# Kernel optimization log

Hardware: AMD Instinct MI355X
Metric: run time of the kernel (lower is better)

## Reference

```python
import jax, jax.numpy as jnp
import numpy as np

# Config (from init_kwargs 'knn')
QUEUE_SIZE = 65536   # K
FEAT_DIM = 256       # D
BATCH = 512          # N (eval_sampling = 1.0 -> all samples used)
NUM_KNNS = 200
NUM_CLASSES = 1000
TEMPERATURE = 0.07


def _l2norm(x):
    return x / jnp.sqrt(jnp.sum(x * x, axis=-1, keepdims=True) + 1e-12)


def setup_inputs() -> dict:
    key = jax.random.key(0)
    k1, k2, k3, k4 = jax.random.split(key, 4)
    features = _l2norm(jax.random.normal(k1, (BATCH, FEAT_DIM), jnp.float32))
    labels = jax.random.randint(k2, (BATCH,), 0, NUM_CLASSES, jnp.int32)
    queue_features = _l2norm(jax.random.normal(k3, (QUEUE_SIZE, FEAT_DIM), jnp.float32))
    queue_labels = jax.random.randint(k4, (QUEUE_SIZE,), 0, NUM_CLASSES, jnp.int32)
    return {
        "features": features,
        "labels": labels,
        "queue_features": queue_features,
        "queue_labels": queue_labels,
        "queue_ptr": 0,
    }


def reference(features, labels, queue_features, queue_labels, queue_ptr):
    # ---- kNN accuracy (train branch, eval_sampling=1.0) ----
    sim = jnp.einsum('nc,kc->nk', features, queue_features)           # [N, K]
    sim_w, sim_idx = jax.lax.top_k(sim, k=NUM_KNNS)                   # [N, Kn]
    sim_w = jnp.exp(sim_w / TEMPERATURE)
    sim_labels = queue_labels[sim_idx]                                # [N, Kn] (vmapped gather)
    # weighted one-hot vote, expressed as a scatter-add (same math,
    # avoids the [N, Kn, C] one-hot intermediate)
    n = features.shape[0]
    pred_scores = jnp.zeros((n, NUM_CLASSES), sim_w.dtype)
    pred_scores = pred_scores.at[jnp.arange(n)[:, None], sim_labels].add(sim_w)
    pred_labels = jnp.argmax(pred_scores, axis=-1)
    accuracy = jnp.mean((pred_labels == labels).astype(jnp.float32))

    # ---- queue update (single device: all_gather == identity) ----
    batch_size = features.shape[0]
    inds = (jnp.arange(batch_size) + queue_ptr) % QUEUE_SIZE  # original asserts divisibility
    new_queue_features = queue_features.at[inds].set(features)
    new_queue_labels = queue_labels.at[inds].set(labels)
    new_queue_ptr = (queue_ptr + batch_size) % QUEUE_SIZE

    return accuracy, new_queue_features, new_queue_labels, new_queue_ptr
```

## Files before the change

kernel.cpp:

```cpp
#include <hip/hip_runtime.h>
#include <math.h>

#define NQ     65536
#define DIM    256
#define NBATCH 512
#define KNN    200
#define NCLS   1000
#define TSELF  0.155f
#define TSELH  0.150f
#define EPSF   0.0041f

#define GM  128
#define GK  32
#define NTN (NQ / GM)
#define KSTEPS (DIM / GK)

typedef unsigned short u16;
typedef unsigned long long u64;
typedef __attribute__((ext_vector_type(8))) short short8;
typedef __attribute__((ext_vector_type(4))) float f32x4;


__device__ __forceinline__ u16 f2bf(float x) {
  unsigned u = __float_as_uint(x);
  return (u16)((u + 0x7FFFu + ((u >> 16) & 1u)) >> 16);
}
__device__ __forceinline__ void load_lds16(const void* g, void* l) {
  __builtin_amdgcn_global_load_lds(
      (const __attribute__((address_space(1))) unsigned int*)g,
      (__attribute__((address_space(3))) unsigned int*)l, 16, 0, 0);
}
__device__ __forceinline__ void store_f4u(float* p, float4 v) {
  p[0] = v.x;
  *(float2*)(p + 1) = make_float2(v.y, v.z);
  p[3] = v.w;
}

__global__ __launch_bounds__(256) void prep_copy_kernel(
    const float* __restrict__ feat, const int* __restrict__ labels,
    const float* __restrict__ qf, const int* __restrict__ ql,
    const int* __restrict__ qptr,
    u16* __restrict__ Bb, u16* __restrict__ Ab,
    int* __restrict__ flag, float* __restrict__ out)
{
  const int idx = blockIdx.x * 256 + threadIdx.x;
  const int ptr = qptr[0];
  const long long NFEAT = (long long)NQ * DIM;

  {
    float4 qv = ((const float4*)qf)[idx];
    int row = idx >> 6;
    int c4  = idx & 63;
    int d = (row - ptr) & (NQ - 1);
    float4 ov = qv;
    if (d < NBATCH) ov = ((const float4*)feat)[d * 64 + c4];
    store_f4u(out + 1 + 4 * (long long)idx, ov);

    ushort4 h;
    h.x = f2bf(qv.x); h.y = f2bf(qv.y); h.z = f2bf(qv.z); h.w = f2bf(qv.w);
    ((ushort4*)Bb)[idx] = h;
  }

  if (idx < NBATCH * DIM / 4) {
    float4 v = ((const float4*)feat)[idx];
    ushort4 h;
    h.x = f2bf(v.x); h.y = f2bf(v.y); h.z = f2bf(v.z); h.w = f2bf(v.w);
    ((ushort4*)Ab)[idx] = h;
  }

  if (idx < NQ) {
    int d = (idx - ptr) & (NQ - 1);
    int v = (d < NBATCH) ? labels[d] : ql[idx];
    out[1 + NFEAT + idx] = (float)v;
  }

  if (idx < NBATCH) flag[idx] = 0;
  if (idx == 0) {
    out[0] = 0.0f;
    out[1 + NFEAT + NQ] = (float)((ptr + NBATCH) & (NQ - 1));
  }
}

__global__ __launch_bounds__(256) void gemm_mfma(
    const u16* __restrict__ A, const u16* __restrict__ B,
    uint2* __restrict__ cand, int* __restrict__ cnt2,
    int* __restrict__ flag, int SLOT)
{
  __shared__ u16 sA[2][GM][GK];
  __shared__ u16 sB[2][GM][GK];
  __shared__ int lcnt[GM];

  const int tid  = threadIdx.x;
  const int wave = tid >> 6, lane = tid & 63;
  const int d  = blockIdx.x;
  const int bm = (d >> 3) & 3;
  const int bn = (d & 7) | ((d >> 5) << 3);

  for (int i = tid; i < GM; i += 256) lcnt[i] = 0;

  const u16* srcBase = ((wave < 2) ? (A + (size_t)bm * GM * DIM)
                                   : (B + (size_t)bn * GM * DIM))
                       + (size_t)(wave & 1) * 64 * DIM;
  const int kx = ((lane & 3) ^ ((lane >> 3) & 3)) * 8;
  const u16* src = srcBase + (lane >> 2) * DIM + kx;
  u16* dst0 = ((wave < 2) ? &sA[0][0][0] : &sB[0][0][0]) + (wave & 1) * 64 * GK;
  u16* dst1 = ((wave < 2) ? &sA[1][0][0] : &sB[1][0][0]) + (wave & 1) * 64 * GK;

  const int wm = (wave & 1) * 64, wn = (wave >> 1) * 64;
  const int fr = lane & 15;
  const int fq = lane >> 4;
  const int fqx = fq ^ ((fr >> 1) & 3);

  f32x4 acc[4][4] = {};

  {
    const u16* s = src;
#pragma unroll
    for (int g = 0; g < 4; ++g)
      load_lds16(s + g * 16 * DIM, dst0 + g * 512);
  }
  __syncthreads();

  for (int t = 0; t < KSTEPS; ++t) {
    const int cur = t & 1;
    if (t + 1 < KSTEPS) {
      const u16* s = src + (t + 1) * GK;
      u16* dl = cur ? dst0 : dst1;
#pragma unroll
      for (int g = 0; g < 4; ++g)
        load_lds16(s + g * 16 * DIM, dl + g * 512);
    }

    short8 a[4], b[4];
#pragma unroll
    for (int i = 0; i < 4; ++i) {
      a[i] = *(const short8*)&sA[cur][wm + i * 16 + fr][fqx * 8];
      b[i] = *(const short8*)&sB[cur][wn + i * 16 + fr][fqx * 8];
    }
#pragma unroll
    for (int i = 0; i < 4; ++i)
#pragma unroll
      for (int j = 0; j < 4; ++j)
        acc[i][j] = __builtin_amdgcn_mfma_f32_16x16x32_bf16(a[i], b[j], acc[i][j], 0, 0, 0);

    __syncthreads();
  }

  const int lrow0 = wm + fq * 4;
  const int ccol  = bn * GM + wn + fr;
#pragma unroll
  for (int i = 0; i < 4; ++i)
#pragma unroll
    for (int j = 0; j < 4; ++j)
#pragma unroll
      for (int r = 0; r < 4; ++r) {
        float v = acc[i][j][r];
        if (v > TSELF) {
          int lr  = lrow0 + i * 16 + r;
          int col = ccol + j * 16;
          int p = atomicAdd(&lcnt[lr], 1);
          if (p < SLOT)
            cand[((size_t)(bm * GM + lr) * NTN + bn) * SLOT + p] =
                make_uint2(__float_as_uint(v), (unsigned)col);
          else
            flag[bm * GM + lr] = 1;
        }
      }
  __syncthreads();
  if (tid < GM) {
    int c = lcnt[tid];
    cnt2[(size_t)(bm * GM + tid) * NTN + bn] = c < SLOT ? c : SLOT;
  }
}

#define NBSEL 2048
#define CCAP  2048
#define LCAP  1024
#define NT    512
#define NG    (NT / 8)
#define NWV   (NT / 64)
#define BINW  ((1.001f - TSELH) / (float)NBSEL)

__global__ __launch_bounds__(NT, 4) void select_kernel(
    const uint2* __restrict__ cand, const int* __restrict__ cnt2,
    const int* __restrict__ flag, const int* __restrict__ labels,
    const int* __restrict__ qlab, const float* __restrict__ qf,
    const float* __restrict__ feat, float* __restrict__ out,
    float inv_n, int SLOT)
{
  __shared__ int   hist[NBSEL];
  __shared__ int   seg[NT];
  __shared__ int   wtot[NWV];
  __shared__ float candV[CCAP];
  __shared__ int   candI[CCAP];
  __shared__ float votes[NCLS];
  __shared__ u64   ek[LCAP];
  __shared__ int   lst[LCAP];
  __shared__ float frow[DIM];
  __shared__ int   s_b, s_cnt, s_mb;
  __shared__ float s_chk;
  __shared__ u64   s_best;

  const int tid = threadIdx.x;
  const int row = blockIdx.x;

  bool fb = (flag[row] != 0);

  if (tid < DIM) frow[tid] = feat[(size_t)row * DIM + tid];
  for (int i = tid; i < NBSEL; i += NT) hist[i] = 0;
  for (int c = tid; c < NCLS; c += NT) votes[c] = 0.0f;
  if (tid == 0) { s_b = 0; s_cnt = 0; s_mb = 0; s_best = 0ull; s_chk = -1.0f; }
  __syncthreads();

  if (!fb) {
    const int*   rowcnt  = cnt2 + (size_t)row * NTN;
    const uint2* rowcand = cand + (size_t)row * NTN * SLOT;
    for (int t = tid; t < NTN; t += NT) {
      int c = rowcnt[t];
      if (c > 0) {
        int p = atomicAdd(&s_cnt, c);
        for (int k = 0; k < c; ++k) {
          if (p + k < CCAP) {
            uint2 e = rowcand[(size_t)t * SLOT + k];
            candV[p + k] = __uint_as_float(e.x);
            candI[p + k] = (int)e.y;
          }
        }
      }
    }
    __syncthreads();
    const int n = s_cnt;
    if (n < KNN || n > CCAP) fb = true;
    else {
      const float SSCALE = 1.0f / BINW;
      for (int i = tid; i < n; i += NT) {
        int b = (int)((candV[i] - TSELH) * SSCALE);
        b = b < 0 ? 0 : (b > NBSEL - 1 ? NBSEL - 1 : b);
        atomicAdd(&hist[b], 1);
      }
      __syncthreads();
      {
        int s = 0;
#pragma unroll
        for (int i = 0; i < NBSEL / NT; ++i) s += hist[tid * (NBSEL / NT) + i];
        const int ln = tid & 63, wv = tid >> 6;
        int acc = s;
#pragma unroll
        for (int off = 1; off < 64; off <<= 1) {
          int o = __shfl_down(acc, off, 64);
          if (ln + off < 64) acc += o;
        }
        if (ln == 0) wtot[wv] = acc;
        __syncthreads();
        int addv = 0;
        for (int w = wv + 1; w < NWV; ++w) addv += wtot[w];
        seg[tid] = acc + addv;
      }
      __syncthreads();
      { int run = (tid < NT - 1) ? seg[tid + 1] : 0;
        for (int i = tid * (NBSEL / NT) + NBSEL / NT - 1;
             i >= tid * (NBSEL / NT); --i) {
          run += hist[i];
          if (run >= KNN) { atomicMax(&s_b, i); break; }
        } }
      __syncthreads();
      const int bstarA = s_b;
      const float thresh = TSELH + (float)bstarA * BINW - 2.0f * EPSF;

      for (int i = tid; i < n; i += NT) {
        if (candV[i] >= thresh) {
          int p = atomicAdd(&s_mb, 1);
          if (p < LCAP) lst[p] = i;
        }
      }
      __syncthreads();
      const int nr = s_mb;
      if (nr > LCAP || nr < KNN) fb = true;
      else {
        const int sub = tid & 7;
        const int grp = tid >> 3;
        const float4* fr4 = (const float4*)frow;

        float4 b0[8];
        if (grp < nr) {
          const float4* qr = (const float4*)(qf + (size_t)candI[lst[grp]] * DIM);
#pragma unroll
          for (int it = 0; it < 8; ++it) b0[it] = qr[sub + it * 8];
        }
        for (int k = grp; k < nr; k += NG) {
          const int kn = k + NG;
          float4 b1[8];
          if (kn < nr) {
            const float4* qr = (const float4*)(qf + (size_t)candI[lst[kn]] * DIM);
#pragma unroll
            for (int it = 0; it < 8; ++it) b1[it] = qr[sub + it * 8];
          }
          float p = 0.0f;
#pragma unroll
          for (int it = 0; it < 8; ++it) {
            float4 a = fr4[sub + it * 8];
            p = fmaf(a.x, b0[it].x, p); p = fmaf(a.y, b0[it].y, p);
            p = fmaf(a.z, b0[it].z, p); p = fmaf(a.w, b0[it].w, p);
          }
          p += __shfl_xor(p, 1, 64);
          p += __shfl_xor(p, 2, 64);
          p += __shfl_xor(p, 4, 64);
          if (sub == 0) candV[lst[k]] = p;
#pragma unroll
          for (int it = 0; it < 8; ++it) b0[it] = b1[it];
        }
        __syncthreads();

        for (int e = tid; e < nr; e += NT) {
          int ci = lst[e];
          ek[e] = ((u64)__float_as_uint(candV[ci]) << 32) |
                  (u64)(0xFFFFFFFFu - (unsigned)candI[ci]);
        }
        __syncthreads();

        for (int e = tid; e < nr; e += NT) {
          u64 ke = ek[e];
          int rank = 0;
          for (int j = 0; j < nr; ++j) rank += (ek[j] > ke);
          if (rank < KNN) {
            float v = __uint_as_float((unsigned)(ke >> 32));
            int col = (int)(0xFFFFFFFFu - (unsigned)(ke & 0xFFFFFFFFull));
            atomicAdd(&votes[qlab[col]], expf(v * (1.0f / 0.07f)));
            if (rank == KNN - 1) s_chk = v;
          }
        }
        __syncthreads();
        if (s_chk < TSELF + EPSF) fb = true;
      }
    }
  }

  if (fb) {
    for (int i = tid; i < NBSEL; i += NT) hist[i] = 0;
    if (tid == 0) { s_b = 0; s_cnt = 0; }
    __syncthreads();

    for (int q = tid; q < NQ; q += NT) {
      const float4* qr = (const float4*)(qf + (size_t)q * DIM);
      const float4* fr = (const float4*)frow;
      float s = 0.0f;
#pragma unroll
      for (int t = 0; t < DIM / 4; ++t) {
        float4 a = fr[t], b = qr[t];
        s = fmaf(a.x, b.x, s); s = fmaf(a.y, b.y, s);
        s = fmaf(a.z, b.z, s); s = fmaf(a.w, b.w, s);
      }
      int bin = (int)((s + 1.0f) * (NBSEL * 0.5f));
      bin = bin < 0 ? 0 : (bin > NBSEL - 1 ? NBSEL - 1 : bin);
      atomicAdd(&hist[bin], 1);
    }
    __syncthreads();

    { int s = 0;
#pragma unroll
      for (int i = 0; i < NBSEL / NT; ++i) s += hist[tid * (NBSEL / NT) + i];
      seg[tid] = s; }
    __syncthreads();
    for (int off = 1; off < NT; off <<= 1) {
      int t = (tid + off < NT) ? seg[tid + off] : 0;
      __syncthreads();
      seg[tid] += t;
      __syncthreads();
    }
    { int run = (tid < NT - 1) ? seg[tid + 1] : 0;
      for (int i = tid * (NBSEL / NT) + NBSEL / NT - 1;
           i >= tid * (NBSEL / NT); --i) {
        run += hist[i];
        if (run >= KNN) { atomicMax(&s_b, i); break; }
      } }
    __syncthreads();
    const int bstar = s_b;

    for (int q = tid; q < NQ; q += NT) {
      const float4* qr = (const float4*)(qf + (size_t)q * DIM);
      const float4* fr = (const float4*)frow;
      float s = 0.0f;
#pragma unroll
      for (int t = 0; t < DIM / 4; ++t) {
        float4 a = fr[t], b = qr[t];
        s = fmaf(a.x, b.x, s); s = fmaf(a.y, b.y, s);
        s = fmaf(a.z, b.z, s); s = fmaf(a.w, b.w, s);
      }
      int bin = (int)((s + 1.0f) * (NBSEL * 0.5f));
      bin = bin < 0 ? 0 : (bin > NBSEL - 1 ? NBSEL - 1 : bin);
      if (bin >= bstar) {
        int p = atomicAdd(&s_cnt, 1);
        if (p < CCAP) { candV[p] = s; candI[p] = q; }
      }
    }
    __syncthreads();
    int m = s_cnt < CCAP ? s_cnt : CCAP;

    int P = 256; while (P < m) P <<= 1;
    for (int i = tid; i < P; i += NT)
      if (i >= m) { candV[i] = -INFINITY; candI[i] = 0x7fffffff; }
    __syncthreads();
    for (int k = 2; k <= P; k <<= 1) {
      for (int j = k >> 1; j > 0; j >>= 1) {
        for (int i = tid; i < P; i += NT) {
          int ixj = i ^ j;
          if (ixj > i) {
            float va = candV[i], vb = candV[ixj];
            int ia = candI[i], ib = candI[ixj];
            bool aFirst = (va > vb) || (va == vb && ia < ib);
            bool up = ((i & k) == 0);
            if (up ? !aFirst : aFirst) {
              candV[i] = vb; candV[ixj] = va;
              candI[i] = ib; candI[ixj] = ia;
            }
          }
        }
        __syncthreads();
      }
    }

    for (int c = tid; c < NCLS; c += NT) votes[c] = 0.0f;
    __syncthreads();
    for (int i = tid; i < KNN; i += NT)
      atomicAdd(&votes[qlab[candI[i]]], expf(candV[i] * (1.0f / 0.07f)));
    __syncthreads();
  }

  u64 key = 0ull;
  for (int c = tid; c < NCLS; c += NT) {
    u64 k2 = ((u64)__float_as_uint(votes[c]) << 32) |
             (u64)(0xFFFFFFFFu - (unsigned)c);
    if (k2 > key) key = k2;
  }
  for (int off = 32; off > 0; off >>= 1) {
    u64 o = __shfl_down(key, off, 64);
    if (o > key) key = o;
  }
  if ((tid & 63) == 0) atomicMax(&s_best, key);
  __syncthreads();
  if (tid == 0) {
    int cls = (int)(0xFFFFFFFFu - (unsigned)(s_best & 0xFFFFFFFFull));
    if (cls == labels[row]) atomicAdd(out, inv_n);
  }
}

extern "C" void kernel_launch(void* const* d_in, const int* in_sizes, int n_in,
                              void* d_out, int out_size, void* d_ws, size_t ws_size,
                              hipStream_t stream)
{
  const float* features = (const float*)d_in[0];
  const int*   labels   = (const int*)d_in[1];
  const float* qfeat    = (const float*)d_in[2];
  const int*   qlab     = (const int*)d_in[3];
  const int*   qptr     = (const int*)d_in[4];
  float* out = (float*)d_out;

  int nbatch = in_sizes[0] / DIM;
  float inv_n = 1.0f / (float)nbatch;

  size_t bBytes = (size_t)NQ * DIM * 2;
  size_t fixed  = bBytes + (size_t)NBATCH * NTN * 4 + NBATCH * 4 +
                  (size_t)NBATCH * DIM * 2;
  int SLOT = 16;
  while ((size_t)NBATCH * NTN * SLOT * 8 + fixed > ws_size && SLOT > 2) SLOT >>= 1;

  u16*   Bb   = (u16*)d_ws;
  uint2* cand = (uint2*)((char*)d_ws + bBytes);
  int*   cnt2 = (int*)((char*)cand + (size_t)NBATCH * NTN * SLOT * 8);
  int*   flagp = cnt2 + (size_t)NBATCH * NTN;
  u16*   Ab   = (u16*)(flagp + NBATCH);

  prep_copy_kernel<<<NQ * DIM / 4 / 256, 256, 0, stream>>>(
      features, labels, qfeat, qlab, qptr, Bb, Ab, flagp, out);

  gemm_mfma<<<(NBATCH / GM) * (NQ / GM), 256, 0, stream>>>(
      Ab, Bb, cand, cnt2, flagp, SLOT);

  select_kernel<<<nbatch, NT, 0, stream>>>(cand, cnt2, flagp, labels, qlab,
                                           qfeat, features, out, inv_n, SLOT);
}
```

Before: 202.6 us.

## Replace per-tile candidate slots with per-row global atomic candidate lists

The GEMM epilogue now appends candidates above threshold straight into one contiguous per-row buffer via a global atomic counter. This replaces the per-tile shared-memory counters, the fixed slot arrays, the per-tile count array and the overflow flag. The select kernel then reads a dense candidate list instead of scanning 512 tile counts and gathering scattered slots, which cuts its gather work and workspace traffic. In exchange, the GEMM epilogue issues global atomics contended across tiles, and candidate order becomes nondeterministic (ties are still broken by index).

```diff
diff --git a/kernel.cpp b/kernel.cpp
--- a/kernel.cpp
+++ b/kernel.cpp
@@ -14,6 +14,7 @@
 #define GK  32
 #define NTN (NQ / GM)
 #define KSTEPS (DIM / GK)
+#define CAND_CAP 2048
 
 typedef unsigned short u16;
 typedef unsigned long long u64;
@@ -41,7 +42,7 @@
     const float* __restrict__ qf, const int* __restrict__ ql,
     const int* __restrict__ qptr,
     u16* __restrict__ Bb, u16* __restrict__ Ab,
-    int* __restrict__ flag, float* __restrict__ out)
+    int* __restrict__ gcnt, float* __restrict__ out)
 {
   const int idx = blockIdx.x * 256 + threadIdx.x;
   const int ptr = qptr[0];
@@ -74,7 +75,7 @@
     out[1 + NFEAT + idx] = (float)v;
   }
 
-  if (idx < NBATCH) flag[idx] = 0;
+  if (idx < NBATCH) gcnt[idx] = 0;
   if (idx == 0) {
     out[0] = 0.0f;
     out[1 + NFEAT + NQ] = (float)((ptr + NBATCH) & (NQ - 1));
@@ -83,20 +84,16 @@
 
 __global__ __launch_bounds__(256) void gemm_mfma(
     const u16* __restrict__ A, const u16* __restrict__ B,
-    uint2* __restrict__ cand, int* __restrict__ cnt2,
-    int* __restrict__ flag, int SLOT)
+    uint2* __restrict__ cand, int* __restrict__ gcnt)
 {
   __shared__ u16 sA[2][GM][GK];
   __shared__ u16 sB[2][GM][GK];
-  __shared__ int lcnt[GM];
 
   const int tid  = threadIdx.x;
   const int wave = tid >> 6, lane = tid & 63;
   const int d  = blockIdx.x;
   const int bm = (d >> 3) & 3;
   const int bn = (d & 7) | ((d >> 5) << 3);
-
-  for (int i = tid; i < GM; i += 256) lcnt[i] = 0;
 
   const u16* srcBase = ((wave < 2) ? (A + (size_t)bm * GM * DIM)
                                    : (B + (size_t)bn * GM * DIM))
@@ -146,7 +143,7 @@
     __syncthreads();
   }
 
-  const int lrow0 = wm + fq * 4;
+  const int lrow0 = bm * GM + wm + fq * 4;
   const int ccol  = bn * GM + wn + fr;
 #pragma unroll
   for (int i = 0; i < 4; ++i)
@@ -156,21 +153,14 @@
       for (int r = 0; r < 4; ++r) {
         float v = acc[i][j][r];
         if (v > TSELF) {
-          int lr  = lrow0 + i * 16 + r;
-          int col = ccol + j * 16;
-          int p = atomicAdd(&lcnt[lr], 1);
-          if (p < SLOT)
-            cand[((size_t)(bm * GM + lr) * NTN + bn) * SLOT + p] =
+          int grow = lrow0 + i * 16 + r;
+          int col  = ccol + j * 16;
+          int p = atomicAdd(&gcnt[grow], 1);
+          if (p < CAND_CAP)
+            cand[(size_t)grow * CAND_CAP + p] =
                 make_uint2(__float_as_uint(v), (unsigned)col);
-          else
-            flag[bm * GM + lr] = 1;
         }
       }
-  __syncthreads();
-  if (tid < GM) {
-    int c = lcnt[tid];
-    cnt2[(size_t)(bm * GM + tid) * NTN + bn] = c < SLOT ? c : SLOT;
-  }
 }
 
 #define NBSEL 2048
@@ -182,11 +172,11 @@
 #define BINW  ((1.001f - TSELH) / (float)NBSEL)
 
 __global__ __launch_bounds__(NT, 4) void select_kernel(
-    const uint2* __restrict__ cand, const int* __restrict__ cnt2,
-    const int* __restrict__ flag, const int* __restrict__ labels,
+    const uint2* __restrict__ cand, const int* __restrict__ gcnt,
+    const int* __restrict__ labels,
     const int* __restrict__ qlab, const float* __restrict__ qf,
     const float* __restrict__ feat, float* __restrict__ out,
-    float inv_n, int SLOT)
+    float inv_n)
 {
   __shared__ int   hist[NBSEL];
   __shared__ int   seg[NT];
@@ -204,134 +194,127 @@
   const int tid = threadIdx.x;
   const int row = blockIdx.x;
 
-  bool fb = (flag[row] != 0);
+  bool fb = false;
 
   if (tid < DIM) frow[tid] = feat[(size_t)row * DIM + tid];
   for (int i = tid; i < NBSEL; i += NT) hist[i] = 0;
   for (int c = tid; c < NCLS; c += NT) votes[c] = 0.0f;
-  if (tid == 0) { s_b = 0; s_cnt = 0; s_mb = 0; s_best = 0ull; s_chk = -1.0f; }
+  if (tid == 0) {
+    s_b = 0; s_mb = 0; s_best = 0ull; s_chk = -1.0f;
+    s_cnt = gcnt[row];
+  }
   __syncthreads();
 
-  if (!fb) {
-    const int*   rowcnt  = cnt2 + (size_t)row * NTN;
-    const uint2* rowcand = cand + (size_t)row * NTN * SLOT;
-    for (int t = tid; t < NTN; t += NT) {
-      int c = rowcnt[t];
-      if (c > 0) {
-        int p = atomicAdd(&s_cnt, c);
-        for (int k = 0; k < c; ++k) {
-          if (p + k < CCAP) {
-            uint2 e = rowcand[(size_t)t * SLOT + k];
-            candV[p + k] = __uint_as_float(e.x);
-            candI[p + k] = (int)e.y;
-          }
+  const int n = s_cnt;
+  if (n < KNN || n > CCAP) fb = true;
+  else {
+    const uint2* rowc = cand + (size_t)row * CAND_CAP;
+    for (int i = tid; i < n; i += NT) {
+      uint2 e = rowc[i];
+      candV[i] = __uint_as_float(e.x);
+      candI[i] = (int)e.y;
+    }
+    __syncthreads();
+
+    const float SSCALE = 1.0f / BINW;
+    for (int i = tid; i < n; i += NT) {
+      int b = (int)((candV[i] - TSELH) * SSCALE);
+      b = b < 0 ? 0 : (b > NBSEL - 1 ? NBSEL - 1 : b);
+      atomicAdd(&hist[b], 1);
+    }
+    __syncthreads();
+    {
+      int s = 0;
+#pragma unroll
+      for (int i = 0; i < NBSEL / NT; ++i) s += hist[tid * (NBSEL / NT) + i];
+      const int ln = tid & 63, wv = tid >> 6;
+      int acc = s;
+#pragma unroll
+      for (int off = 1; off < 64; off <<= 1) {
+        int o = __shfl_down(acc, off, 64);
+        if (ln + off < 64) acc += o;
+      }
+      if (ln == 0) wtot[wv] = acc;
+      __syncthreads();
+      int addv = 0;
+      for (int w = wv + 1; w < NWV; ++w) addv += wtot[w];
+      seg[tid] = acc + addv;
+    }
+    __syncthreads();
+    { int run = (tid < NT - 1) ? seg[tid + 1] : 0;
+      for (int i = tid * (NBSEL / NT) + NBSEL / NT - 1;
+           i >= tid * (NBSEL / NT); --i) {
+        run += hist[i];
+        if (run >= KNN) { atomicMax(&s_b, i); break; }
+      } }
+    __syncthreads();
+    const int bstarA = s_b;
+    const float thresh = TSELH + (float)bstarA * BINW - 2.0f * EPSF;
+
+    for (int i = tid; i < n; i += NT) {
+      if (candV[i] >= thresh) {
+        int p = atomicAdd(&s_mb, 1);
+        if (p < LCAP) lst[p] = i;
+      }
+    }
+    __syncthreads();
+    const int nr = s_mb;
+    if (nr > LCAP || nr < KNN) fb = true;
+    else {
+      const int sub = tid & 7;
+      const int grp = tid >> 3;
+      const float4* fr4 = (const float4*)frow;
+
+      float4 b0[8];
+      if (grp < nr) {
+        const float4* qr = (const float4*)(qf + (size_t)candI[lst[grp]] * DIM);
+#pragma unroll
+        for (int it = 0; it < 8; ++it) b0[it] = qr[sub + it * 8];
+      }
+      for (int k = grp; k < nr; k += NG) {
+        const int kn = k + NG;
+        float4 b1[8];
+        if (kn < nr) {
+          const float4* qr = (const float4*)(qf + (size_t)candI[lst[kn]] * DIM);
+#pragma unroll
+          for (int it = 0; it < 8; ++it) b1[it] = qr[sub + it * 8];
         }
-      }
-    }
-    __syncthreads();
-    const int n = s_cnt;
-    if (n < KNN || n > CCAP) fb = true;
-    else {
-      const float SSCALE = 1.0f / BINW;
-      for (int i = tid; i < n; i += NT) {
-        int b = (int)((candV[i] - TSELH) * SSCALE);
-        b = b < 0 ? 0 : (b > NBSEL - 1 ? NBSEL - 1 : b);
-        atomicAdd(&hist[b], 1);
-      }
-      __syncthreads();
-      {
-        int s = 0;
-#pragma unroll
-        for (int i = 0; i < NBSEL / NT; ++i) s += hist[tid * (NBSEL / NT) + i];
-        const int ln = tid & 63, wv = tid >> 6;
-        int acc = s;
-#pragma unroll
-        for (int off = 1; off < 64; off <<= 1) {
-          int o = __shfl_down(acc, off, 64);
-          if (ln + off < 64) acc += o;
+        float p = 0.0f;
+#pragma unroll
+        for (int it = 0; it < 8; ++it) {
+          float4 a = fr4[sub + it * 8];
+          p = fmaf(a.x, b0[it].x, p); p = fmaf(a.y, b0[it].y, p);
+          p = fmaf(a.z, b0[it].z, p); p = fmaf(a.w, b0[it].w, p);
         }
-        if (ln == 0) wtot[wv] = acc;
-        __syncthreads();
-        int addv = 0;
-        for (int w = wv + 1; w < NWV; ++w) addv += wtot[w];
-        seg[tid] = acc + addv;
-      }
-      __syncthreads();
-      { int run = (tid < NT - 1) ? seg[tid + 1] : 0;
-        for (int i = tid * (NBSEL / NT) + NBSEL / NT - 1;
-             i >= tid * (NBSEL / NT); --i) {
-          run += hist[i];
-          if (run >= KNN) { atomicMax(&s_b, i); break; }
-        } }
-      __syncthreads();
-      const int bstarA = s_b;
-      const float thresh = TSELH + (float)bstarA * BINW - 2.0f * EPSF;
-
-      for (int i = tid; i < n; i += NT) {
-        if (candV[i] >= thresh) {
-          int p = atomicAdd(&s_mb, 1);
-          if (p < LCAP) lst[p] = i;
+        p += __shfl_xor(p, 1, 64);
+        p += __shfl_xor(p, 2, 64);
+        p += __shfl_xor(p, 4, 64);
+        if (sub == 0) candV[lst[k]] = p;
+#pragma unroll
+        for (int it = 0; it < 8; ++it) b0[it] = b1[it];
+      }
+      __syncthreads();
+
+      for (int e = tid; e < nr; e += NT) {
+        int ci = lst[e];
+        ek[e] = ((u64)__float_as_uint(candV[ci]) << 32) |
+                (u64)(0xFFFFFFFFu - (unsigned)candI[ci]);
+      }
+      __syncthreads();
+
+      for (int e = tid; e < nr; e += NT) {
+        u64 ke = ek[e];
+        int rank = 0;
+        for (int j = 0; j < nr; ++j) rank += (ek[j] > ke);
+        if (rank < KNN) {
+          float v = __uint_as_float((unsigned)(ke >> 32));
+          int col = (int)(0xFFFFFFFFu - (unsigned)(ke & 0xFFFFFFFFull));
+          atomicAdd(&votes[qlab[col]], expf(v * (1.0f / 0.07f)));
+          if (rank == KNN - 1) s_chk = v;
         }
       }
       __syncthreads();
-      const int nr = s_mb;
-      if (nr > LCAP || nr < KNN) fb = true;
-      else {
-        const int sub = tid & 7;
-        const int grp = tid >> 3;
-        const float4* fr4 = (const float4*)frow;
-
-        float4 b0[8];
-        if (grp < nr) {
-          const float4* qr = (const float4*)(qf + (size_t)candI[lst[grp]] * DIM);
-#pragma unroll
-          for (int it = 0; it < 8; ++it) b0[it] = qr[sub + it * 8];
-        }
-        for (int k = grp; k < nr; k += NG) {
-          const int kn = k + NG;
-          float4 b1[8];
-          if (kn < nr) {
-            const float4* qr = (const float4*)(qf + (size_t)candI[lst[kn]] * DIM);
-#pragma unroll
-            for (int it = 0; it < 8; ++it) b1[it] = qr[sub + it * 8];
-          }
-          float p = 0.0f;
-#pragma unroll
-          for (int it = 0; it < 8; ++it) {
-            float4 a = fr4[sub + it * 8];
-            p = fmaf(a.x, b0[it].x, p); p = fmaf(a.y, b0[it].y, p);
-            p = fmaf(a.z, b0[it].z, p); p = fmaf(a.w, b0[it].w, p);
-          }
-          p += __shfl_xor(p, 1, 64);
-          p += __shfl_xor(p, 2, 64);
-          p += __shfl_xor(p, 4, 64);
-          if (sub == 0) candV[lst[k]] = p;
-#pragma unroll
-          for (int it = 0; it < 8; ++it) b0[it] = b1[it];
-        }
-        __syncthreads();
-
-        for (int e = tid; e < nr; e += NT) {
-          int ci = lst[e];
-          ek[e] = ((u64)__float_as_uint(candV[ci]) << 32) |
-                  (u64)(0xFFFFFFFFu - (unsigned)candI[ci]);
-        }
-        __syncthreads();
-
-        for (int e = tid; e < nr; e += NT) {
-          u64 ke = ek[e];
-          int rank = 0;
-          for (int j = 0; j < nr; ++j) rank += (ek[j] > ke);
-          if (rank < KNN) {
-            float v = __uint_as_float((unsigned)(ke >> 32));
-            int col = (int)(0xFFFFFFFFu - (unsigned)(ke & 0xFFFFFFFFull));
-            atomicAdd(&votes[qlab[col]], expf(v * (1.0f / 0.07f)));
-            if (rank == KNN - 1) s_chk = v;
-          }
-        }
-        __syncthreads();
-        if (s_chk < TSELF + EPSF) fb = true;
-      }
+      if (s_chk < TSELF + EPSF) fb = true;
     }
   }
 
@@ -459,23 +442,17 @@
   float inv_n = 1.0f / (float)nbatch;
 
   size_t bBytes = (size_t)NQ * DIM * 2;
-  size_t fixed  = bBytes + (size_t)NBATCH * NTN * 4 + NBATCH * 4 +
-                  (size_t)NBATCH * DIM * 2;
-  int SLOT = 16;
-  while ((size_t)NBATCH * NTN * SLOT * 8 + fixed > ws_size && SLOT > 2) SLOT >>= 1;
-
   u16*   Bb   = (u16*)d_ws;
   uint2* cand = (uint2*)((char*)d_ws + bBytes);
-  int*   cnt2 = (int*)((char*)cand + (size_t)NBATCH * NTN * SLOT * 8);
-  int*   flagp = cnt2 + (size_t)NBATCH * NTN;
-  u16*   Ab   = (u16*)(flagp + NBATCH);
+  int*   gcnt = (int*)((char*)cand + (size_t)NBATCH * CAND_CAP * 8);
+  u16*   Ab   = (u16*)(gcnt + NBATCH);
 
   prep_copy_kernel<<<NQ * DIM / 4 / 256, 256, 0, stream>>>(
-      features, labels, qfeat, qlab, qptr, Bb, Ab, flagp, out);
+      features, labels, qfeat, qlab, qptr, Bb, Ab, gcnt, out);
 
   gemm_mfma<<<(NBATCH / GM) * (NQ / GM), 256, 0, stream>>>(
-      Ab, Bb, cand, cnt2, flagp, SLOT);
-
-  select_kernel<<<nbatch, NT, 0, stream>>>(cand, cnt2, flagp, labels, qlab,
-                                           qfeat, features, out, inv_n, SLOT);
-}
+      Ab, Bb, cand, gcnt);
+
+  select_kernel<<<nbatch, NT, 0, stream>>>(cand, gcnt, labels, qlab,
+                                           qfeat, features, out, inv_n);
+}
```

Result: slower. 318.9 us (+57.4%).
